# Optimization experiments

Hardware: AMD Instinct MI355X
Metric: run time of the kernel (lower is better)

Reference implementation:

```python
import jax, jax.numpy as jnp
import numpy as np

ALPHA = 20.0 / 100.0  # dt / tau


def setup_inputs() -> dict:
    key = jax.random.key(0)
    k1, k2, k3, k4 = jax.random.split(key, 4)
    B, T, I, H = 128, 4096, 128, 512
    inputs = jax.random.normal(k1, (B, T, I), dtype=jnp.float32)
    hidden = jnp.zeros((B, H), dtype=jnp.float32)
    w_in = jax.random.normal(k2, (H, I), dtype=jnp.float32) / np.sqrt(I)
    w_rec = jax.random.normal(k3, (H, H), dtype=jnp.float32) / np.sqrt(H)
    b_rec = jnp.zeros((H,), dtype=jnp.float32)
    w_out = jax.random.normal(k4, (1, H), dtype=jnp.float32) * (2.0 / np.sqrt(H))
    b_out = jnp.zeros((1,), dtype=jnp.float32)
    return {"inputs": inputs, "hidden": hidden, "w_in": w_in, "w_rec": w_rec,
            "b_rec": b_rec, "w_out": w_out, "b_out": b_out}


def reference(inputs, hidden, w_in, w_rec, b_rec, w_out, b_out):
    # inputs: (B, T, I); hidden: (B, H)
    # Precompute input projection for all timesteps (batched GEMM).
    inp_proj = jnp.einsum('bti,hi->tbh', inputs, w_in)  # (T, B, H)

    def step(h, x_t):
        rec = jnp.einsum('bh,gh->bg', h, w_rec) + b_rec  # w_rec @ h per Linear
        activated = jax.nn.relu(x_t + rec)
        h_new = (1.0 - ALPHA) * h + ALPHA * activated
        return h_new, h_new

    h_final, states = jax.lax.scan(step, hidden, inp_proj)  # states: (T, B, H)
    # Linear readout at every timestep: y(t) = w_out h(t) + b_out, squeezed.
    outputs = jnp.einsum('tbh,oh->bto', states, w_out)[..., 0] + b_out[0]  # (B, T)
    return outputs, h_final
```

## Files before the change

### kernel.cpp

```cpp
#include <hip/hip_runtime.h>
#include <hip/hip_bf16.h>

#define B_ 128
#define T_ 4096
#define I_ 128
#define H_ 512

typedef __attribute__((ext_vector_type(8))) short short8;
typedef __attribute__((ext_vector_type(4))) float f32x4;
typedef __attribute__((ext_vector_type(4))) unsigned short us4;

__device__ __forceinline__ unsigned short f2bf(float f) {
  union { float f; unsigned int u; } v; v.f = f;
  unsigned int r = v.u + 0x7FFFu + ((v.u >> 16) & 1u);
  return (unsigned short)(r >> 16);
}

__device__ __forceinline__ short8 cvt8(f32x4 a, f32x4 b) {
  union { short8 s; unsigned short u[8]; } r;
#pragma unroll
  for (int j = 0; j < 4; ++j) { r.u[j] = f2bf(a[j]); r.u[4 + j] = f2bf(b[j]); }
  return r.s;
}

#define WBF_BYTES ((size_t)(H_ * H_ + H_ * I_) * 2)
#define CNT_OFF   WBF_BYTES
#define HX_OFF    (CNT_OFF + 32)
#define HX_BYTES  ((size_t)8 * 2 * 16 * H_ * 2)
#define YP_OFF    (((HX_OFF + HX_BYTES) + 63) & ~(size_t)63)
#define YP_BYTES  ((size_t)8 * T_ * 8 * 16 * 4)
#define WS_NEED   (YP_OFF + YP_BYTES)

__global__ void cvt_w_kernel(const float* __restrict__ w_rec,
                             const float* __restrict__ w_in,
                             unsigned short* __restrict__ wbf,
                             unsigned int* __restrict__ cnt) {
  int i = blockIdx.x * blockDim.x + threadIdx.x;
  if (i < H_ * H_) wbf[i] = f2bf(w_rec[i]);
  if (i < H_ * I_) wbf[H_ * H_ + i] = f2bf(w_in[i]);
  if (cnt != nullptr && i < 8) cnt[i] = 0;
}

__global__ __launch_bounds__(256, 1)
void rnn_pair_kernel(const float* __restrict__ inputs,
                     const float* __restrict__ hidden,
                     const float* __restrict__ b_rec,
                     const float* __restrict__ w_out,
                     const unsigned short* __restrict__ wbf,
                     unsigned short* __restrict__ hx,
                     unsigned int* __restrict__ cnt,
                     float* __restrict__ ypartial,
                     float* __restrict__ hfin) {
  const int tid  = threadIdx.x;
  const int wave = tid >> 6;
  const int lane = tid & 63;
  const int q    = lane >> 4;
  const int c    = lane & 15;
  const int pair = blockIdx.x & 7;
  const int half = blockIdx.x >> 3;
  const int wip  = half * 4 + wave;
  const int r0   = pair * 16;
  const int n0   = half * 256 + wave * 64;

  short8 wr[16][4], wi[4][4];
  {
    const unsigned short* wrp = wbf + (size_t)(n0 + c) * H_ + q * 8;
    const unsigned short* wip_ = wbf + (size_t)H_ * H_ + (size_t)(n0 + c) * I_ + q * 8;
#pragma unroll
    for (int kk = 0; kk < 16; ++kk)
#pragma unroll
      for (int nt = 0; nt < 4; ++nt)
        wr[kk][nt] = *(const short8*)(wrp + (size_t)nt * 16 * H_ + kk * 32);
#pragma unroll
    for (int kk = 0; kk < 4; ++kk)
#pragma unroll
      for (int nt = 0; nt < 4; ++nt)
        wi[kk][nt] = *(const short8*)(wip_ + (size_t)nt * 16 * I_ + kk * 32);
  }

  f32x4 hreg[4], brec[4], wout[4];
#pragma unroll
  for (int nt = 0; nt < 4; ++nt)
#pragma unroll
    for (int r = 0; r < 4; ++r) {
      const int g = n0 + nt * 16 + q * 4 + r;
      hreg[nt][r] = hidden[(size_t)(r0 + c) * H_ + g];
      brec[nt][r] = b_rec[g];
      wout[nt][r] = w_out[g];
    }

  unsigned int* mycnt = cnt + pair;
  unsigned short* hx0 = hx + (size_t)(pair * 2) * 16 * H_;
  unsigned short* hx1 = hx0 + 16 * H_;

  const float* xbase = inputs + (size_t)(r0 + c) * T_ * I_ + q * 8;

  f32x4 xn[4][2];
#pragma unroll
  for (int kk = 0; kk < 4; ++kk) {
    xn[kk][0] = *(const f32x4*)(xbase + kk * 32);
    xn[kk][1] = *(const f32x4*)(xbase + kk * 32 + 4);
  }

#pragma unroll
  for (int nt = 0; nt < 4; ++nt) {
    us4 hb;
#pragma unroll
    for (int r = 0; r < 4; ++r) hb[r] = f2bf(hreg[nt][r]);
    *(us4*)(hx0 + (size_t)c * H_ + n0 + nt * 16 + q * 4) = hb;
  }
  if (lane == 0)
    __hip_atomic_fetch_add(mycnt, 1u, __ATOMIC_RELEASE, __HIP_MEMORY_SCOPE_AGENT);

  for (int t = 0; t < T_; ++t) {
    const unsigned target = 8u * (unsigned)(t + 1);
    while (__hip_atomic_load(mycnt, __ATOMIC_ACQUIRE, __HIP_MEMORY_SCOPE_AGENT) < target) {}

    short8 xc[4];
#pragma unroll
    for (int kk = 0; kk < 4; ++kk) xc[kk] = cvt8(xn[kk][0], xn[kk][1]);
    {
      const float* xp = xbase + (size_t)((t + 1 < T_) ? (t + 1) : t) * I_;
#pragma unroll
      for (int kk = 0; kk < 4; ++kk) {
        xn[kk][0] = *(const f32x4*)(xp + kk * 32);
        xn[kk][1] = *(const f32x4*)(xp + kk * 32 + 4);
      }
    }

    const unsigned short* hr = ((t & 1) ? hx1 : hx0) + (size_t)c * H_ + q * 8;

    f32x4 acc[4];
#pragma unroll
    for (int nt = 0; nt < 4; ++nt) acc[nt] = (f32x4){0.f, 0.f, 0.f, 0.f};

    short8 hb4[4];
#pragma unroll
    for (int kk = 0; kk < 4; ++kk) hb4[kk] = *(const short8*)(hr + kk * 32);
#pragma unroll
    for (int kk = 0; kk < 16; ++kk) {
      short8 b = hb4[kk & 3];
      if (kk < 12) hb4[kk & 3] = *(const short8*)(hr + (kk + 4) * 32);
#pragma unroll
      for (int nt = 0; nt < 4; ++nt)
        acc[nt] = __builtin_amdgcn_mfma_f32_16x16x32_bf16(wr[kk][nt], b, acc[nt], 0, 0, 0);
    }
#pragma unroll
    for (int kk = 0; kk < 4; ++kk)
#pragma unroll
      for (int nt = 0; nt < 4; ++nt)
        acc[nt] = __builtin_amdgcn_mfma_f32_16x16x32_bf16(wi[kk][nt], xc[kk], acc[nt], 0, 0, 0);

    float yl = 0.f;
    unsigned short* hw = (t & 1) ? hx0 : hx1;
#pragma unroll
    for (int nt = 0; nt < 4; ++nt) {
      us4 hb;
#pragma unroll
      for (int r = 0; r < 4; ++r) {
        float act = fmaxf(acc[nt][r] + brec[nt][r], 0.f);
        float h = hreg[nt][r] * 0.8f + 0.2f * act;
        hreg[nt][r] = h;
        hb[r] = f2bf(h);
        yl = __builtin_fmaf(wout[nt][r], h, yl);
      }
      if (t + 1 < T_)
        *(us4*)(hw + (size_t)c * H_ + n0 + nt * 16 + q * 4) = hb;
    }
    yl += __shfl_xor(yl, 16, 64);
    yl += __shfl_xor(yl, 32, 64);
    if (q == 0)
      ypartial[(((size_t)pair * T_ + t) * 8 + wip) * 16 + c] = yl;

    if (t + 1 < T_ && lane == 0)
      __hip_atomic_fetch_add(mycnt, 1u, __ATOMIC_RELEASE, __HIP_MEMORY_SCOPE_AGENT);
  }

#pragma unroll
  for (int nt = 0; nt < 4; ++nt)
    *(f32x4*)(hfin + (size_t)(r0 + c) * H_ + n0 + nt * 16 + q * 4) = hreg[nt];
}

__global__ void reduce_y_kernel(const float* __restrict__ ypartial,
                                const float* __restrict__ b_out,
                                float* __restrict__ out) {
  const int idx = blockIdx.x * 256 + threadIdx.x;
  const int t = idx & (T_ - 1);
  const int r = idx >> 12;
  const int p = r >> 4, b = r & 15;
  const float* yp = ypartial + (((size_t)p * T_ + t) * 8) * 16 + b;
  float s = b_out[0];
#pragma unroll
  for (int w = 0; w < 8; ++w) s += yp[w * 16];
  out[(size_t)r * T_ + t] = s;
}

template <bool WBF16>
__global__ __launch_bounds__(512, 2)
void rnn_kernel_fb(const float* __restrict__ inputs,
                   const float* __restrict__ hidden,
                   const float* __restrict__ w_in_f,
                   const float* __restrict__ w_rec_f,
                   const float* __restrict__ b_rec,
                   const float* __restrict__ w_out,
                   const float* __restrict__ b_out,
                   const unsigned short* __restrict__ wbf,
                   float* __restrict__ out) {
  __shared__ alignas(16) unsigned short hs[2][16][520];
  __shared__ alignas(16) float ypart[2][8][16];

  const int tid  = threadIdx.x;
  const int wave = tid >> 6;
  const int lane = tid & 63;
  const int q    = lane >> 4;
  const int c    = lane & 15;
  const int r0   = blockIdx.x * 16;
  const int n0   = wave * 64;

  for (int e = tid; e < 16 * H_; e += 512) {
    int rr = e >> 9, cc = e & (H_ - 1);
    hs[0][rr][cc] = f2bf(hidden[(size_t)(r0 + rr) * H_ + cc]);
  }

  f32x4 hreg[4];
  float brec[4], wout[4];
#pragma unroll
  for (int nt = 0; nt < 4; ++nt) {
    const int col = n0 + nt * 16 + c;
    brec[nt] = b_rec[col];
    wout[nt] = w_out[col];
#pragma unroll
    for (int r = 0; r < 4; ++r)
      hreg[nt][r] = hidden[(size_t)(r0 + q * 4 + r) * H_ + col];
  }
  const float bout = b_out[0];
  __syncthreads();

  const unsigned short* wrecb = wbf;
  const unsigned short* winb  = wbf + H_ * H_;
  const size_t wr_off = (size_t)(n0 + c) * H_ + q * 8;
  const size_t wi_off = (size_t)(n0 + c) * I_ + q * 8;
  const float* xbase = inputs + (size_t)(r0 + c) * T_ * I_ + q * 8;

#pragma unroll 2
  for (int t = 0; t < T_; ++t) {
    const int rb = t & 1, wb = rb ^ 1;
    f32x4 xf[4][2];
    const float* xp = xbase + (size_t)t * I_;
#pragma unroll
    for (int kk = 0; kk < 4; ++kk) {
      xf[kk][0] = *(const f32x4*)(xp + kk * 32);
      xf[kk][1] = *(const f32x4*)(xp + kk * 32 + 4);
    }
    f32x4 acc[4];
#pragma unroll
    for (int nt = 0; nt < 4; ++nt) acc[nt] = (f32x4){0.f, 0.f, 0.f, 0.f};
    const unsigned short* hrow = &hs[rb][c][q * 8];
#pragma unroll
    for (int kk = 0; kk < 16; ++kk) {
      short8 a = *(const short8*)(hrow + kk * 32);
#pragma unroll
      for (int nt = 0; nt < 4; ++nt) {
        short8 b;
        if constexpr (WBF16) {
          b = *(const short8*)(wrecb + wr_off + (size_t)nt * 16 * H_ + kk * 32);
        } else {
          const float* p = w_rec_f + wr_off + (size_t)nt * 16 * H_ + kk * 32;
          b = cvt8(*(const f32x4*)p, *(const f32x4*)(p + 4));
        }
        acc[nt] = __builtin_amdgcn_mfma_f32_16x16x32_bf16(a, b, acc[nt], 0, 0, 0);
      }
    }
#pragma unroll
    for (int kk = 0; kk < 4; ++kk) {
      short8 ax = cvt8(xf[kk][0], xf[kk][1]);
#pragma unroll
      for (int nt = 0; nt < 4; ++nt) {
        short8 b;
        if constexpr (WBF16) {
          b = *(const short8*)(winb + wi_off + (size_t)nt * 16 * I_ + kk * 32);
        } else {
          const float* p = w_in_f + wi_off + (size_t)nt * 16 * I_ + kk * 32;
          b = cvt8(*(const f32x4*)p, *(const f32x4*)(p + 4));
        }
        acc[nt] = __builtin_amdgcn_mfma_f32_16x16x32_bf16(ax, b, acc[nt], 0, 0, 0);
      }
    }
    float yp2[4] = {0.f, 0.f, 0.f, 0.f};
#pragma unroll
    for (int nt = 0; nt < 4; ++nt) {
#pragma unroll
      for (int r = 0; r < 4; ++r) {
        float act = fmaxf(acc[nt][r] + brec[nt], 0.f);
        float h = hreg[nt][r] * 0.8f + 0.2f * act;
        hreg[nt][r] = h;
        hs[wb][q * 4 + r][n0 + nt * 16 + c] = f2bf(h);
        yp2[r] = __builtin_fmaf(wout[nt], h, yp2[r]);
      }
    }
#pragma unroll
    for (int off = 8; off >= 1; off >>= 1) {
#pragma unroll
      for (int r = 0; r < 4; ++r) yp2[r] += __shfl_xor(yp2[r], off, 64);
    }
    if (c == 0)
      *(f32x4*)&ypart[wb][wave][q * 4] = (f32x4){yp2[0], yp2[1], yp2[2], yp2[3]};
    __syncthreads();
    if (tid < 16) {
      float s = bout;
#pragma unroll
      for (int w = 0; w < 8; ++w) s += ypart[wb][w][tid];
      out[(size_t)(r0 + tid) * T_ + t] = s;
    }
  }
  float* hfin = out + (size_t)B_ * T_;
#pragma unroll
  for (int nt = 0; nt < 4; ++nt)
#pragma unroll
    for (int r = 0; r < 4; ++r)
      hfin[(size_t)(r0 + q * 4 + r) * H_ + n0 + nt * 16 + c] = hreg[nt][r];
}

extern "C" void kernel_launch(void* const* d_in, const int* in_sizes, int n_in,
                              void* d_out, int out_size, void* d_ws, size_t ws_size,
                              hipStream_t stream) {
  const float* inputs = (const float*)d_in[0];
  const float* hidden = (const float*)d_in[1];
  const float* w_in   = (const float*)d_in[2];
  const float* w_rec  = (const float*)d_in[3];
  const float* b_rec  = (const float*)d_in[4];
  const float* w_out  = (const float*)d_in[5];
  const float* b_out  = (const float*)d_in[6];
  float* out = (float*)d_out;

  if (ws_size >= WS_NEED) {
    unsigned short* wbf = (unsigned short*)d_ws;
    unsigned int*   cnt = (unsigned int*)((char*)d_ws + CNT_OFF);
    unsigned short* hx  = (unsigned short*)((char*)d_ws + HX_OFF);
    float*          yp  = (float*)((char*)d_ws + YP_OFF);
    float*          hfin = out + (size_t)B_ * T_;
    cvt_w_kernel<<<dim3((H_ * H_ + 255) / 256), dim3(256), 0, stream>>>(w_rec, w_in, wbf, cnt);
    rnn_pair_kernel<<<dim3(16), dim3(256), 0, stream>>>(
        inputs, hidden, b_rec, w_out, wbf, hx, cnt, yp, hfin);
    reduce_y_kernel<<<dim3((B_ * T_) / 256), dim3(256), 0, stream>>>(yp, b_out, out);
  } else if (ws_size >= WBF_BYTES) {
    unsigned short* wbf = (unsigned short*)d_ws;
    cvt_w_kernel<<<dim3((H_ * H_ + 255) / 256), dim3(256), 0, stream>>>(w_rec, w_in, wbf, nullptr);
    rnn_kernel_fb<true><<<dim3(8), dim3(512), 0, stream>>>(
        inputs, hidden, w_in, w_rec, b_rec, w_out, b_out, wbf, out);
  } else {
    rnn_kernel_fb<false><<<dim3(8), dim3(512), 0, stream>>>(
        inputs, hidden, w_in, w_rec, b_rec, w_out, b_out, (const unsigned short*)nullptr, out);
  }
}
```

Before: 31.62 ms.

## Relax inter-block sync with atomic h exchange and overlap input MFMAs before wait

Replaces acquire/release atomics on the per-pair step counter with relaxed atomics plus explicit vmcnt waits. The hidden-state exchange buffer is now read and written through relaxed agent-scope atomic 64-bit loads and stores, which avoids the cache flush and invalidate that acquire/release semantics imply. The input-projection MFMAs are moved ahead of the spin-wait so they overlap the wait for other blocks. The next timestep's input prefetch is moved after the counter increment, taking it off the critical path before publishing. The risk is memory-ordering correctness, since visibility now depends on the relaxed atomics and the waitcnt.

```diff
diff --git a/kernel.cpp b/kernel.cpp
--- a/kernel.cpp
+++ b/kernel.cpp
@@ -21,6 +21,20 @@
 #pragma unroll
   for (int j = 0; j < 4; ++j) { r.u[j] = f2bf(a[j]); r.u[4 + j] = f2bf(b[j]); }
   return r.s;
+}
+
+__device__ __forceinline__ short8 ld_h16(const unsigned short* p) {
+  union { short8 s; unsigned long long u[2]; } r;
+  r.u[0] = __hip_atomic_load((const unsigned long long*)p,
+                             __ATOMIC_RELAXED, __HIP_MEMORY_SCOPE_AGENT);
+  r.u[1] = __hip_atomic_load((const unsigned long long*)(p + 4),
+                             __ATOMIC_RELAXED, __HIP_MEMORY_SCOPE_AGENT);
+  return r.s;
+}
+__device__ __forceinline__ void st_h8(unsigned short* p, us4 v) {
+  union { us4 v; unsigned long long u; } r; r.v = v;
+  __hip_atomic_store((unsigned long long*)p, r.u,
+                     __ATOMIC_RELAXED, __HIP_MEMORY_SCOPE_AGENT);
 }
 
 #define WBF_BYTES ((size_t)(H_ * H_ + H_ * I_) * 2)
@@ -38,7 +52,8 @@
   int i = blockIdx.x * blockDim.x + threadIdx.x;
   if (i < H_ * H_) wbf[i] = f2bf(w_rec[i]);
   if (i < H_ * I_) wbf[H_ * H_ + i] = f2bf(w_in[i]);
-  if (cnt != nullptr && i < 8) cnt[i] = 0;
+  if (cnt != nullptr && i < 8)
+    __hip_atomic_store(&cnt[i], 0u, __ATOMIC_RELAXED, __HIP_MEMORY_SCOPE_AGENT);
 }
 
 __global__ __launch_bounds__(256, 1)
@@ -107,52 +122,48 @@
     us4 hb;
 #pragma unroll
     for (int r = 0; r < 4; ++r) hb[r] = f2bf(hreg[nt][r]);
-    *(us4*)(hx0 + (size_t)c * H_ + n0 + nt * 16 + q * 4) = hb;
-  }
+    st_h8(hx0 + (size_t)c * H_ + n0 + nt * 16 + q * 4, hb);
+  }
+  asm volatile("s_waitcnt vmcnt(0)" ::: "memory");
   if (lane == 0)
-    __hip_atomic_fetch_add(mycnt, 1u, __ATOMIC_RELEASE, __HIP_MEMORY_SCOPE_AGENT);
+    __hip_atomic_fetch_add(mycnt, 1u, __ATOMIC_RELAXED, __HIP_MEMORY_SCOPE_AGENT);
 
   for (int t = 0; t < T_; ++t) {
+    short8 xc[4];
+#pragma unroll
+    for (int kk = 0; kk < 4; ++kk) xc[kk] = cvt8(xn[kk][0], xn[kk][1]);
+    f32x4 acc[4];
+#pragma unroll
+    for (int nt = 0; nt < 4; ++nt) acc[nt] = (f32x4){0.f, 0.f, 0.f, 0.f};
+#pragma unroll
+    for (int kk = 0; kk < 4; ++kk)
+#pragma unroll
+      for (int nt = 0; nt < 4; ++nt)
+        acc[nt] = __builtin_amdgcn_mfma_f32_16x16x32_bf16(wi[kk][nt], xc[kk], acc[nt], 0, 0, 0);
+
+    __builtin_amdgcn_sched_barrier(0);
+
     const unsigned target = 8u * (unsigned)(t + 1);
-    while (__hip_atomic_load(mycnt, __ATOMIC_ACQUIRE, __HIP_MEMORY_SCOPE_AGENT) < target) {}
-
-    short8 xc[4];
-#pragma unroll
-    for (int kk = 0; kk < 4; ++kk) xc[kk] = cvt8(xn[kk][0], xn[kk][1]);
-    {
-      const float* xp = xbase + (size_t)((t + 1 < T_) ? (t + 1) : t) * I_;
-#pragma unroll
-      for (int kk = 0; kk < 4; ++kk) {
-        xn[kk][0] = *(const f32x4*)(xp + kk * 32);
-        xn[kk][1] = *(const f32x4*)(xp + kk * 32 + 4);
-      }
-    }
+    while (__hip_atomic_load(mycnt, __ATOMIC_RELAXED, __HIP_MEMORY_SCOPE_AGENT) < target) {}
+    asm volatile("" ::: "memory");
 
     const unsigned short* hr = ((t & 1) ? hx1 : hx0) + (size_t)c * H_ + q * 8;
 
-    f32x4 acc[4];
-#pragma unroll
-    for (int nt = 0; nt < 4; ++nt) acc[nt] = (f32x4){0.f, 0.f, 0.f, 0.f};
-
     short8 hb4[4];
 #pragma unroll
-    for (int kk = 0; kk < 4; ++kk) hb4[kk] = *(const short8*)(hr + kk * 32);
+    for (int kk = 0; kk < 4; ++kk) hb4[kk] = ld_h16(hr + kk * 32);
 #pragma unroll
     for (int kk = 0; kk < 16; ++kk) {
       short8 b = hb4[kk & 3];
-      if (kk < 12) hb4[kk & 3] = *(const short8*)(hr + (kk + 4) * 32);
+      if (kk < 12) hb4[kk & 3] = ld_h16(hr + (kk + 4) * 32);
 #pragma unroll
       for (int nt = 0; nt < 4; ++nt)
         acc[nt] = __builtin_amdgcn_mfma_f32_16x16x32_bf16(wr[kk][nt], b, acc[nt], 0, 0, 0);
     }
-#pragma unroll
-    for (int kk = 0; kk < 4; ++kk)
-#pragma unroll
-      for (int nt = 0; nt < 4; ++nt)
-        acc[nt] = __builtin_amdgcn_mfma_f32_16x16x32_bf16(wi[kk][nt], xc[kk], acc[nt], 0, 0, 0);
-
+
+    const bool pub = (t + 1 < T_);
+    unsigned short* hw = (t & 1) ? hx0 : hx1;
     float yl = 0.f;
-    unsigned short* hw = (t & 1) ? hx0 : hx1;
 #pragma unroll
     for (int nt = 0; nt < 4; ++nt) {
       us4 hb;
@@ -164,16 +175,26 @@
         hb[r] = f2bf(h);
         yl = __builtin_fmaf(wout[nt][r], h, yl);
       }
-      if (t + 1 < T_)
-        *(us4*)(hw + (size_t)c * H_ + n0 + nt * 16 + q * 4) = hb;
-    }
+      if (pub) st_h8(hw + (size_t)c * H_ + n0 + nt * 16 + q * 4, hb);
+    }
+    if (pub) {
+      asm volatile("s_waitcnt vmcnt(0)" ::: "memory");
+      if (lane == 0)
+        __hip_atomic_fetch_add(mycnt, 1u, __ATOMIC_RELAXED, __HIP_MEMORY_SCOPE_AGENT);
+    }
+
     yl += __shfl_xor(yl, 16, 64);
     yl += __shfl_xor(yl, 32, 64);
     if (q == 0)
       ypartial[(((size_t)pair * T_ + t) * 8 + wip) * 16 + c] = yl;
-
-    if (t + 1 < T_ && lane == 0)
-      __hip_atomic_fetch_add(mycnt, 1u, __ATOMIC_RELEASE, __HIP_MEMORY_SCOPE_AGENT);
+    {
+      const float* xp = xbase + (size_t)((t + 1 < T_) ? (t + 1) : t) * I_;
+#pragma unroll
+      for (int kk = 0; kk < 4; ++kk) {
+        xn[kk][0] = *(const f32x4*)(xp + kk * 32);
+        xn[kk][1] = *(const f32x4*)(xp + kk * 32 + 4);
+      }
+    }
   }
 
 #pragma unroll
```

Measured after the change: 28.90 ms. 8.6% less time.
